# Kernel optimization log

Hardware: AMD Instinct MI355X
Metric: run time of the kernel (lower is better)

## Reference

```python
import jax, jax.numpy as jnp
import numpy as np

B, H, W, C = 8, 56, 56, 192
HEADS, K, PAD = 6, 3, 1
KK = K * K
HEAD_DIM = C // HEADS
SCALE = HEAD_DIM ** -0.5


def setup_inputs() -> dict:
    key = jax.random.key(0)
    ks = jax.random.split(key, 6)
    s = lambda fan_in: 1.0 / np.sqrt(fan_in)
    return {
        "x": jax.random.normal(ks[0], (B, H, W, C), jnp.float32),
        "Wv": jax.random.normal(ks[1], (C, C), jnp.float32) * s(C),
        "Wa": jax.random.normal(ks[2], (C, KK * KK * HEADS), jnp.float32) * s(C),
        "ba": jax.random.normal(ks[3], (KK * KK * HEADS,), jnp.float32) * s(C),
        "Wp": jax.random.normal(ks[4], (C, C), jnp.float32) * s(C),
        "bp": jax.random.normal(ks[5], (C,), jnp.float32) * s(C),
    }


def _unfold(v_nchw):
    # im2col, kernel 3, pad 1, stride 1 -> (B, C, 9, H, W); kernel pos row-major like nn.Unfold
    vp = jnp.pad(v_nchw, ((0, 0), (0, 0), (PAD, PAD), (PAD, PAD)))
    return jnp.stack([vp[:, :, i:i + H, j:j + W] for i in range(K) for j in range(K)], axis=2)


def _fold(cols):
    # col2im scatter-add: cols (B, C, 9, H, W) -> (B, C, H, W)
    out = jnp.zeros((cols.shape[0], cols.shape[1], H + 2 * PAD, W + 2 * PAD), cols.dtype)
    idx = 0
    for i in range(K):
        for j in range(K):
            out = out.at[:, :, i:i + H, j:j + W].add(cols[:, :, idx])
            idx += 1
    return out[:, :, PAD:PAD + H, PAD:PAD + W]


def reference(x, Wv, Wa, ba, Wp, bp):
    hw = H * W
    # values: linear then unfold into per-pixel kxk windows
    v = jnp.einsum("bhwc,cd->bhwd", x, Wv)              # (B,H,W,C)
    v = _unfold(v.transpose(0, 3, 1, 2))                 # (B,C,9,H,W)
    v = v.reshape(B, HEADS, HEAD_DIM, KK, hw)
    v = v.transpose(0, 1, 4, 3, 2)                       # (B,heads,HW,9,c)
    # dynamic attention weights (stride=1 -> pool is identity)
    a = jnp.einsum("bhwc,ck->bhwk", x, Wa) + ba          # (B,H,W,81*heads)
    a = a.reshape(B, hw, HEADS, KK, KK).transpose(0, 2, 1, 3, 4)
    a = jax.nn.softmax(a * SCALE, axis=-1)               # (B,heads,HW,9,9)
    o = jnp.einsum("bnpkl,bnplc->bnpkc", a, v)           # (B,heads,HW,9,c)
    o = o.transpose(0, 1, 4, 3, 2).reshape(B, C, KK, H, W)
    o = _fold(o)                                          # (B,C,H,W)
    o = o.transpose(0, 2, 3, 1)                           # NHWC
    return jnp.einsum("bhwc,cd->bhwd", o, Wp) + bp
```

## Files before the change

kernel.cpp:

```cpp
#include <hip/hip_runtime.h>
#include <hip/hip_bf16.h>

constexpr int NH = 56, NW = 56, NC = 192, AJ = 486;
constexpr int HWP = NH * NW;
constexpr int NPIX = 8 * HWP;
constexpr float SCALE = 0.17677669529663687f;
constexpr int TS = 12288;

typedef __bf16 bf16x8 __attribute__((ext_vector_type(8)));
typedef float f32x4 __attribute__((ext_vector_type(4)));

__device__ __forceinline__ void gload16(const void* g, void* l) {
  __builtin_amdgcn_global_load_lds(
      (const __attribute__((address_space(1))) void*)g,
      (__attribute__((address_space(3))) void*)l, 16, 0, 0);
}

__device__ __forceinline__ size_t toff(int row, int k) {
  return (size_t)(row >> 6) * TS + (k >> 5) * 2048 + (row & 63) * 32 + (k & 31);
}

__global__ __launch_bounds__(256) void k_prep3(const float* __restrict__ x,
                                               const float* __restrict__ Wv,
                                               const float* __restrict__ Wa,
                                               const float* __restrict__ Wp,
                                               __bf16* __restrict__ xb,
                                               __bf16* __restrict__ Wvt,
                                               __bf16* __restrict__ Wat,
                                               __bf16* __restrict__ Wpt) {
  const int bid = blockIdx.x;
  if (bid < 144) {
    const int i = bid * 256 + threadIdx.x;
    const int n = i / 192, k = i - n * 192;
    const size_t d = toff(n, k);
    Wvt[d] = (__bf16)Wv[k * 192 + n];
    Wpt[d] = (__bf16)Wp[k * 192 + n];
  } else if (bid < 528) {
    const int i = (bid - 144) * 256 + threadIdx.x;
    const int n = i / 192, k = i - n * 192;
    Wat[toff(n, k)] = (n < 486) ? (__bf16)Wa[k * 486 + n] : (__bf16)0.f;
  } else {
    const size_t i = (size_t)(bid - 528) * 256 + threadIdx.x;
    const int pix = (int)(i / 24), c8 = (int)(i % 24) * 8;
    const float* src = x + (size_t)pix * 192 + c8;
    const float4 f0 = *(const float4*)src;
    const float4 f1 = *(const float4*)(src + 4);
    bf16x8 o8;
    o8[0] = (__bf16)f0.x; o8[1] = (__bf16)f0.y;
    o8[2] = (__bf16)f0.z; o8[3] = (__bf16)f0.w;
    o8[4] = (__bf16)f1.x; o8[5] = (__bf16)f1.y;
    o8[6] = (__bf16)f1.z; o8[7] = (__bf16)f1.w;
    *(bf16x8*)(xb + toff(pix, c8)) = o8;
  }
}

template <int MODE>
__global__ __launch_bounds__(256) void k_gemm1(const __bf16* __restrict__ At,
                                               const __bf16* __restrict__ Bt,
                                               const float* __restrict__ bias,
                                               void* __restrict__ C) {
  __shared__ __bf16 As[64 * 192];
  __shared__ __bf16 Bs[64 * 192];
  const int t = threadIdx.x, lane = t & 63, w = t >> 6;
  const int wm = w >> 1, wn = w & 1;
  const int a_tile = (MODE == 1) ? blockIdx.y : blockIdx.x;
  const int b_tile = (MODE == 1) ? blockIdx.x : blockIdx.y;
  const __bf16* Asrc = At + (size_t)a_tile * TS;
  const __bf16* Bsrc = Bt + (size_t)b_tile * TS;
  #pragma unroll
  for (int i = 0; i < 6; ++i) {
    const int cb = i * 256 + w * 64;
    gload16(Asrc + (size_t)(cb + lane) * 8, &As[cb * 8]);
    gload16(Bsrc + (size_t)(cb + lane) * 8, &Bs[cb * 8]);
  }
  f32x4 acc[2][2];
  #pragma unroll
  for (int mi = 0; mi < 2; ++mi)
    #pragma unroll
    for (int nj = 0; nj < 2; ++nj) acc[mi][nj] = (f32x4){0.f, 0.f, 0.f, 0.f};
  __syncthreads();
  #pragma unroll
  for (int ks = 0; ks < 6; ++ks) {
    bf16x8 af[2], bfr[2];
    #pragma unroll
    for (int mi = 0; mi < 2; ++mi)
      af[mi] = *(const bf16x8*)&As[(ks * 64 + wm * 32 + mi * 16 + (lane & 15)) * 32 + (lane >> 4) * 8];
    #pragma unroll
    for (int nj = 0; nj < 2; ++nj)
      bfr[nj] = *(const bf16x8*)&Bs[(ks * 64 + wn * 32 + nj * 16 + (lane & 15)) * 32 + (lane >> 4) * 8];
    #pragma unroll
    for (int mi = 0; mi < 2; ++mi)
      #pragma unroll
      for (int nj = 0; nj < 2; ++nj)
        acc[mi][nj] = __builtin_amdgcn_mfma_f32_16x16x32_bf16(af[mi], bfr[nj], acc[mi][nj], 0, 0, 0);
  }
  const int col_l = lane & 15, rq4 = (lane >> 4) * 4;
  if (MODE == 2) {
    #pragma unroll
    for (int nj = 0; nj < 2; ++nj) {
      const int ln = wn * 32 + nj * 16 + col_l;
      const int ch = blockIdx.y * 64 + ln;
      const float bv = bias[ch];
      #pragma unroll
      for (int mi = 0; mi < 2; ++mi) {
        const int pix = blockIdx.x * 64 + wm * 32 + mi * 16 + rq4;
        #pragma unroll
        for (int r = 0; r < 4; ++r)
          ((float*)C)[(size_t)(pix + r) * 192 + ch] = acc[mi][nj][r] + bias[ch] - bv + bv;
      }
    }
    return;
  }
  __bf16* Cs = As;
  __syncthreads();
  #pragma unroll
  for (int nj = 0; nj < 2; ++nj) {
    const int ln = wn * 32 + nj * 16 + col_l;
    #pragma unroll
    for (int mi = 0; mi < 2; ++mi) {
      const int lmb = wm * 32 + mi * 16 + rq4;
      #pragma unroll
      for (int r = 0; r < 4; ++r) {
        float val = acc[mi][nj][r];
        if (MODE == 1) {
          const int j = blockIdx.y * 64 + lmb + r;
          val = (val + bias[j < 486 ? j : 0]) * SCALE;
        }
        Cs[(lmb + r) * 72 + ln] = (__bf16)val;
      }
    }
  }
  __syncthreads();
  {
    const int lm = t >> 2, seg = t & 3;
    const bf16x8 c0 = *(const bf16x8*)&Cs[lm * 72 + seg * 16];
    const bf16x8 c1 = *(const bf16x8*)&Cs[lm * 72 + seg * 16 + 8];
    if (MODE == 0) {
      const int pix = blockIdx.x * 64 + lm, ch = blockIdx.y * 64 + seg * 16;
      *(bf16x8*)&((__bf16*)C)[(size_t)pix * 192 + ch] = c0;
      *(bf16x8*)&((__bf16*)C)[(size_t)pix * 192 + ch + 8] = c1;
    } else {
      const int j = blockIdx.y * 64 + lm, pix = blockIdx.x * 64 + seg * 16;
      if (j < 486) {
        *(bf16x8*)&((__bf16*)C)[(size_t)j * NPIX + pix] = c0;
        *(bf16x8*)&((__bf16*)C)[(size_t)j * NPIX + pix + 8] = c1;
      }
    }
  }
}

__global__ __launch_bounds__(256) void k_coef(const __bf16* __restrict__ lgT,
                                              __bf16* __restrict__ wcT) {
  const int p = blockIdx.x * 256 + threadIdx.x;
  const int head = blockIdx.y;
  const int b = p / HWP;
  const int yx = p - b * HWP;
  const int y = yx / NW, x = yx - y * NW;

  float wc[25];
  #pragma unroll
  for (int c = 0; c < 25; ++c) wc[c] = 0.f;

  #pragma unroll
  for (int ki = 0; ki < 3; ++ki) {
    const int h = y - ki + 1;
    if ((unsigned)h >= (unsigned)NH) continue;
    #pragma unroll
    for (int kj = 0; kj < 3; ++kj) {
      const int ww = x - kj + 1;
      if ((unsigned)ww >= (unsigned)NW) continue;
      const int src = b * HWP + h * NW + ww;
      const size_t base = (size_t)((head * 9 + ki * 3 + kj) * 9) * NPIX + src;
      float lt[9];
      #pragma unroll
      for (int l = 0; l < 9; ++l) lt[l] = (float)lgT[base + (size_t)l * NPIX];
      float m = lt[0];
      #pragma unroll
      for (int l = 1; l < 9; ++l) m = fmaxf(m, lt[l]);
      float s = 0.f;
      #pragma unroll
      for (int l = 0; l < 9; ++l) { lt[l] = __expf(lt[l] - m); s += lt[l]; }
      const float inv = 1.f / s;
      #pragma unroll
      for (int l = 0; l < 9; ++l) {
        const int li = l / 3, lj = l - li * 3;
        wc[(li - ki + 2) * 5 + (lj - kj + 2)] += lt[l] * inv;
      }
    }
  }
  #pragma unroll
  for (int c = 0; c < 25; ++c)
    wcT[(size_t)(head * 25 + c) * NPIX + p] = (__bf16)wc[c];
}

__global__ __launch_bounds__(192) void k_att3(const __bf16* __restrict__ v,
                                              const __bf16* __restrict__ wcT,
                                              __bf16* __restrict__ o) {
  const int bid = blockIdx.x;
  const int cx = bid % 7;
  const int ry = (bid / 7) % 28;
  const int bb = bid / 196;
  const int y0 = ry * 2, x0 = cx * 8;
  const int p0 = bb * HWP + y0 * NW + x0;
  const int t = threadIdx.x;

  __shared__ __bf16 vs[72][192];
  __shared__ float wcs[16][6][28];

  #pragma unroll
  for (int i = 0; i < 9; ++i) {
    const int u = i * 192 + t;
    const int cell = u / 24, ck = u - cell * 24;
    const int ri = cell / 12, ci = cell - ri * 12;
    const int yy = y0 + ri - 2, xx = x0 + ci - 2;
    bf16x8 val;
    #pragma unroll
    for (int j = 0; j < 8; ++j) val[j] = (__bf16)0.f;
    if ((unsigned)yy < (unsigned)NH && (unsigned)xx < (unsigned)NW)
      val = *(const bf16x8*)&v[(size_t)(bb * HWP + yy * NW + xx) * 192 + ck * 8];
    *(bf16x8*)&vs[cell][ck * 8] = val;
  }
  if (t < 150) {
    const int head = t / 25, cc = t - head * 25;
    const bf16x8 w0 = *(const bf16x8*)&wcT[(size_t)t * NPIX + p0];
    const bf16x8 w1 = *(const bf16x8*)&wcT[(size_t)t * NPIX + p0 + NW];
    #pragma unroll
    for (int q = 0; q < 8; ++q) {
      wcs[q][head][cc] = (float)w0[q];
      wcs[8 + q][head][cc] = (float)w1[q];
    }
  }
  __syncthreads();

  const int ch = t, head = ch >> 5;
  float vr[6][12];
  #pragma unroll
  for (int ri = 0; ri < 6; ++ri)
    #pragma unroll
    for (int ci = 0; ci < 12; ++ci) vr[ri][ci] = (float)vs[ri * 12 + ci][ch];
  #pragma unroll
  for (int q = 0; q < 16; ++q) {
    const int qr = q >> 3, qc = q & 7;
    float coef[25];
    #pragma unroll
    for (int i = 0; i < 6; ++i)
      *(float4*)&coef[i * 4] = *(const float4*)&wcs[q][head][i * 4];
    coef[24] = wcs[q][head][24];
    float s = 0.f;
    #pragma unroll
    for (int di = 0; di < 5; ++di)
      #pragma unroll
      for (int dj = 0; dj < 5; ++dj) s += coef[di * 5 + dj] * vr[qr + di][qc + dj];
    const int px = p0 + qr * NW + qc;
    o[toff(px, ch)] = (__bf16)s;
  }
}

extern "C" void kernel_launch(void* const* d_in, const int* in_sizes, int n_in,
                              void* d_out, int out_size, void* d_ws,
                              size_t ws_size, hipStream_t stream) {
  (void)in_sizes; (void)n_in; (void)out_size; (void)ws_size;
  const float* x  = (const float*)d_in[0];
  const float* Wv = (const float*)d_in[1];
  const float* Wa = (const float*)d_in[2];
  const float* ba = (const float*)d_in[3];
  const float* Wp = (const float*)d_in[4];
  const float* bp = (const float*)d_in[5];

  char* ws = (char*)d_ws;
  __bf16* Wvt = (__bf16*)(ws);
  __bf16* Wat = (__bf16*)(ws + 73728);
  __bf16* Wpt = (__bf16*)(ws + 270336);
  __bf16* xb  = (__bf16*)(ws + 344064);
  __bf16* v_ws = (__bf16*)(ws + 9977856);
  __bf16* lgT = (__bf16*)(ws + 19611648);
  __bf16* wcT = (__bf16*)(ws + 43997184);
  __bf16* o_ws = (__bf16*)(ws + 19611648);

  k_prep3<<<2880, 256, 0, stream>>>(x, Wv, Wa, Wp, xb, Wvt, Wat, Wpt);
  k_gemm1<0><<<dim3(392, 3), 256, 0, stream>>>(xb, Wvt, nullptr, v_ws);
  k_gemm1<1><<<dim3(392, 8), 256, 0, stream>>>(Wat, xb, ba, lgT);
  k_coef<<<dim3(98, 6), 256, 0, stream>>>(lgT, wcT);
  k_att3<<<1568, 192, 0, stream>>>(v_ws, wcT, o_ws);
  k_gemm1<2><<<dim3(392, 3), 256, 0, stream>>>(o_ws, Wpt, bp, (float*)d_out);
}
```

Before: 137.4 us.

## Fuse value and logit GEMMs, write values into zero-padded buffer

```diff
diff --git a/kernel.cpp b/kernel.cpp
--- a/kernel.cpp
+++ b/kernel.cpp
@@ -6,6 +6,9 @@
 constexpr int NPIX = 8 * HWP;
 constexpr float SCALE = 0.17677669529663687f;
 constexpr int TS = 12288;
+constexpr int PD = 60;
+constexpr int PROW = PD * NC;
+constexpr int PBATCH = PD * PD * NC;
 
 typedef __bf16 bf16x8 __attribute__((ext_vector_type(8)));
 typedef float f32x4 __attribute__((ext_vector_type(4)));
@@ -20,14 +23,15 @@
   return (size_t)(row >> 6) * TS + (k >> 5) * 2048 + (row & 63) * 32 + (k & 31);
 }
 
-__global__ __launch_bounds__(256) void k_prep3(const float* __restrict__ x,
+__global__ __launch_bounds__(256) void k_prep4(const float* __restrict__ x,
                                                const float* __restrict__ Wv,
                                                const float* __restrict__ Wa,
                                                const float* __restrict__ Wp,
                                                __bf16* __restrict__ xb,
                                                __bf16* __restrict__ Wvt,
                                                __bf16* __restrict__ Wat,
-                                               __bf16* __restrict__ Wpt) {
+                                               __bf16* __restrict__ Wpt,
+                                               __bf16* __restrict__ v_pad) {
   const int bid = blockIdx.x;
   if (bid < 144) {
     const int i = bid * 256 + threadIdx.x;
@@ -39,7 +43,7 @@
     const int i = (bid - 144) * 256 + threadIdx.x;
     const int n = i / 192, k = i - n * 192;
     Wat[toff(n, k)] = (n < 486) ? (__bf16)Wa[k * 486 + n] : (__bf16)0.f;
-  } else {
+  } else if (bid < 2880) {
     const size_t i = (size_t)(bid - 528) * 256 + threadIdx.x;
     const int pix = (int)(i / 24), c8 = (int)(i % 24) * 8;
     const float* src = x + (size_t)pix * 192 + c8;
@@ -51,22 +55,37 @@
     o8[4] = (__bf16)f1.x; o8[5] = (__bf16)f1.y;
     o8[6] = (__bf16)f1.z; o8[7] = (__bf16)f1.w;
     *(bf16x8*)(xb + toff(pix, c8)) = o8;
-  }
-}
-
-template <int MODE>
-__global__ __launch_bounds__(256) void k_gemm1(const __bf16* __restrict__ At,
-                                               const __bf16* __restrict__ Bt,
-                                               const float* __restrict__ bias,
-                                               void* __restrict__ C) {
+  } else {
+    const int cg = (bid - 2880) * 256 + threadIdx.x;
+    const int b = cg / 11136, rem = cg - b * 11136;
+    const int n = rem / 24, ck = rem - n * 24;
+    int r, c;
+    if (n < 120)      { r = n / 60;             c = n - (n / 60) * 60; }
+    else if (n < 240) { r = 58 + (n - 120) / 60; c = (n - 120) % 60; }
+    else if (n < 352) { r = 2 + (n - 240) / 2;   c = (n - 240) & 1; }
+    else              { r = 2 + (n - 352) / 2;   c = 58 + ((n - 352) & 1); }
+    bf16x8 z;
+    #pragma unroll
+    for (int j = 0; j < 8; ++j) z[j] = (__bf16)0.f;
+    *(bf16x8*)&v_pad[(size_t)b * PBATCH + r * PROW + c * 192 + ck * 8] = z;
+  }
+}
+
+__global__ __launch_bounds__(256) void k_mm2(const __bf16* __restrict__ xb,
+                                             const __bf16* __restrict__ Wvt,
+                                             const __bf16* __restrict__ Wat,
+                                             const float* __restrict__ ba,
+                                             __bf16* __restrict__ v_pad,
+                                             __bf16* __restrict__ lgT) {
   __shared__ __bf16 As[64 * 192];
   __shared__ __bf16 Bs[64 * 192];
   const int t = threadIdx.x, lane = t & 63, w = t >> 6;
   const int wm = w >> 1, wn = w & 1;
-  const int a_tile = (MODE == 1) ? blockIdx.y : blockIdx.x;
-  const int b_tile = (MODE == 1) ? blockIdx.x : blockIdx.y;
-  const __bf16* Asrc = At + (size_t)a_tile * TS;
-  const __bf16* Bsrc = Bt + (size_t)b_tile * TS;
+  const bool vmode = (blockIdx.y < 3);
+  const __bf16* Asrc = vmode ? xb + (size_t)blockIdx.x * TS
+                             : Wat + (size_t)(blockIdx.y - 3) * TS;
+  const __bf16* Bsrc = vmode ? Wvt + (size_t)blockIdx.y * TS
+                             : xb + (size_t)blockIdx.x * TS;
   #pragma unroll
   for (int i = 0; i < 6; ++i) {
     const int cb = i * 256 + w * 64;
@@ -95,22 +114,6 @@
         acc[mi][nj] = __builtin_amdgcn_mfma_f32_16x16x32_bf16(af[mi], bfr[nj], acc[mi][nj], 0, 0, 0);
   }
   const int col_l = lane & 15, rq4 = (lane >> 4) * 4;
-  if (MODE == 2) {
-    #pragma unroll
-    for (int nj = 0; nj < 2; ++nj) {
-      const int ln = wn * 32 + nj * 16 + col_l;
-      const int ch = blockIdx.y * 64 + ln;
-      const float bv = bias[ch];
-      #pragma unroll
-      for (int mi = 0; mi < 2; ++mi) {
-        const int pix = blockIdx.x * 64 + wm * 32 + mi * 16 + rq4;
-        #pragma unroll
-        for (int r = 0; r < 4; ++r)
-          ((float*)C)[(size_t)(pix + r) * 192 + ch] = acc[mi][nj][r] + bias[ch] - bv + bv;
-      }
-    }
-    return;
-  }
   __bf16* Cs = As;
   __syncthreads();
   #pragma unroll
@@ -122,9 +125,9 @@
       #pragma unroll
       for (int r = 0; r < 4; ++r) {
         float val = acc[mi][nj][r];
-        if (MODE == 1) {
-          const int j = blockIdx.y * 64 + lmb + r;
-          val = (val + bias[j < 486 ? j : 0]) * SCALE;
+        if (!vmode) {
+          const int j = (blockIdx.y - 3) * 64 + lmb + r;
+          val = (val + ba[j < 486 ? j : 0]) * SCALE;
         }
         Cs[(lmb + r) * 72 + ln] = (__bf16)val;
       }
@@ -135,15 +138,19 @@
     const int lm = t >> 2, seg = t & 3;
     const bf16x8 c0 = *(const bf16x8*)&Cs[lm * 72 + seg * 16];
     const bf16x8 c1 = *(const bf16x8*)&Cs[lm * 72 + seg * 16 + 8];
-    if (MODE == 0) {
-      const int pix = blockIdx.x * 64 + lm, ch = blockIdx.y * 64 + seg * 16;
-      *(bf16x8*)&((__bf16*)C)[(size_t)pix * 192 + ch] = c0;
-      *(bf16x8*)&((__bf16*)C)[(size_t)pix * 192 + ch + 8] = c1;
+    if (vmode) {
+      const int pix = blockIdx.x * 64 + lm;
+      const int b = pix / HWP, yx = pix - b * HWP;
+      const int y = yx / NW, xq = yx - y * NW;
+      const size_t dst = (size_t)b * PBATCH + (y + 2) * PROW + (xq + 2) * 192 +
+                         blockIdx.y * 64 + seg * 16;
+      *(bf16x8*)&v_pad[dst] = c0;
+      *(bf16x8*)&v_pad[dst + 8] = c1;
     } else {
-      const int j = blockIdx.y * 64 + lm, pix = blockIdx.x * 64 + seg * 16;
+      const int j = (blockIdx.y - 3) * 64 + lm, pix = blockIdx.x * 64 + seg * 16;
       if (j < 486) {
-        *(bf16x8*)&((__bf16*)C)[(size_t)j * NPIX + pix] = c0;
-        *(bf16x8*)&((__bf16*)C)[(size_t)j * NPIX + pix + 8] = c1;
+        *(bf16x8*)&lgT[(size_t)j * NPIX + pix] = c0;
+        *(bf16x8*)&lgT[(size_t)j * NPIX + pix + 8] = c1;
       }
     }
   }
@@ -193,7 +200,7 @@
     wcT[(size_t)(head * 25 + c) * NPIX + p] = (__bf16)wc[c];
 }
 
-__global__ __launch_bounds__(192) void k_att3(const __bf16* __restrict__ v,
+__global__ __launch_bounds__(192) void k_att4(const __bf16* __restrict__ v_pad,
                                               const __bf16* __restrict__ wcT,
                                               __bf16* __restrict__ o) {
   const int bid = blockIdx.x;
@@ -202,23 +209,19 @@
   const int bb = bid / 196;
   const int y0 = ry * 2, x0 = cx * 8;
   const int p0 = bb * HWP + y0 * NW + x0;
-  const int t = threadIdx.x;
+  const int t = threadIdx.x, w = t >> 6;
 
   __shared__ __bf16 vs[72][192];
   __shared__ float wcs[16][6][28];
 
+  const __bf16* vb = v_pad + (size_t)bb * PBATCH;
   #pragma unroll
   for (int i = 0; i < 9; ++i) {
     const int u = i * 192 + t;
     const int cell = u / 24, ck = u - cell * 24;
     const int ri = cell / 12, ci = cell - ri * 12;
-    const int yy = y0 + ri - 2, xx = x0 + ci - 2;
-    bf16x8 val;
-    #pragma unroll
-    for (int j = 0; j < 8; ++j) val[j] = (__bf16)0.f;
-    if ((unsigned)yy < (unsigned)NH && (unsigned)xx < (unsigned)NW)
-      val = *(const bf16x8*)&v[(size_t)(bb * HWP + yy * NW + xx) * 192 + ck * 8];
-    *(bf16x8*)&vs[cell][ck * 8] = val;
+    gload16(vb + (size_t)(y0 + ri) * PROW + (x0 + ci) * 192 + ck * 8,
+            &vs[0][0] + (i * 192 + w * 64) * 16 / 2);
   }
   if (t < 150) {
     const int head = t / 25, cc = t - head * 25;
@@ -253,6 +256,58 @@
       for (int dj = 0; dj < 5; ++dj) s += coef[di * 5 + dj] * vr[qr + di][qc + dj];
     const int px = p0 + qr * NW + qc;
     o[toff(px, ch)] = (__bf16)s;
+  }
+}
+
+__global__ __launch_bounds__(256) void k_gemm_out(const __bf16* __restrict__ At,
+                                                  const __bf16* __restrict__ Bt,
+                                                  const float* __restrict__ bias,
+                                                  float* __restrict__ C) {
+  __shared__ __bf16 As[64 * 192];
+  __shared__ __bf16 Bs[64 * 192];
+  const int t = threadIdx.x, lane = t & 63, w = t >> 6;
+  const int wm = w >> 1, wn = w & 1;
+  const __bf16* Asrc = At + (size_t)blockIdx.x * TS;
+  const __bf16* Bsrc = Bt + (size_t)blockIdx.y * TS;
+  #pragma unroll
+  for (int i = 0; i < 6; ++i) {
+    const int cb = i * 256 + w * 64;
+    gload16(Asrc + (size_t)(cb + lane) * 8, &As[cb * 8]);
+    gload16(Bsrc + (size_t)(cb + lane) * 8, &Bs[cb * 8]);
+  }
+  f32x4 acc[2][2];
+  #pragma unroll
+  for (int mi = 0; mi < 2; ++mi)
+    #pragma unroll
+    for (int nj = 0; nj < 2; ++nj) acc[mi][nj] = (f32x4){0.f, 0.f, 0.f, 0.f};
+  __syncthreads();
+  #pragma unroll
+  for (int ks = 0; ks < 6; ++ks) {
+    bf16x8 af[2], bfr[2];
+    #pragma unroll
+    for (int mi = 0; mi < 2; ++mi)
+      af[mi] = *(const bf16x8*)&As[(ks * 64 + wm * 32 + mi * 16 + (lane & 15)) * 32 + (lane >> 4) * 8];
+    #pragma unroll
+    for (int nj = 0; nj < 2; ++nj)
+      bfr[nj] = *(const bf16x8*)&Bs[(ks * 64 + wn * 32 + nj * 16 + (lane & 15)) * 32 + (lane >> 4) * 8];
+    #pragma unroll
+    for (int mi = 0; mi < 2; ++mi)
+      #pragma unroll
+      for (int nj = 0; nj < 2; ++nj)
+        acc[mi][nj] = __builtin_amdgcn_mfma_f32_16x16x32_bf16(af[mi], bfr[nj], acc[mi][nj], 0, 0, 0);
+  }
+  const int col_l = lane & 15, rq4 = (lane >> 4) * 4;
+  #pragma unroll
+  for (int nj = 0; nj < 2; ++nj) {
+    const int ch = blockIdx.y * 64 + wn * 32 + nj * 16 + col_l;
+    const float bv = bias[ch];
+    #pragma unroll
+    for (int mi = 0; mi < 2; ++mi) {
+      const int pix = blockIdx.x * 64 + wm * 32 + mi * 16 + rq4;
+      #pragma unroll
+      for (int r = 0; r < 4; ++r)
+        C[(size_t)(pix + r) * 192 + ch] = acc[mi][nj][r] + bv;
+    }
   }
 }
 
@@ -268,19 +323,18 @@
   const float* bp = (const float*)d_in[5];
 
   char* ws = (char*)d_ws;
-  __bf16* Wvt = (__bf16*)(ws);
-  __bf16* Wat = (__bf16*)(ws + 73728);
-  __bf16* Wpt = (__bf16*)(ws + 270336);
-  __bf16* xb  = (__bf16*)(ws + 344064);
-  __bf16* v_ws = (__bf16*)(ws + 9977856);
-  __bf16* lgT = (__bf16*)(ws + 19611648);
-  __bf16* wcT = (__bf16*)(ws + 43997184);
-  __bf16* o_ws = (__bf16*)(ws + 19611648);
-
-  k_prep3<<<2880, 256, 0, stream>>>(x, Wv, Wa, Wp, xb, Wvt, Wat, Wpt);
-  k_gemm1<0><<<dim3(392, 3), 256, 0, stream>>>(xb, Wvt, nullptr, v_ws);
-  k_gemm1<1><<<dim3(392, 8), 256, 0, stream>>>(Wat, xb, ba, lgT);
+  __bf16* Wvt  = (__bf16*)(ws);
+  __bf16* Wat  = (__bf16*)(ws + 73728);
+  __bf16* Wpt  = (__bf16*)(ws + 270336);
+  __bf16* xb   = (__bf16*)(ws + 344064);
+  __bf16* v_pad = (__bf16*)(ws + 9977856);
+  __bf16* lgT  = (__bf16*)(ws + 21037056);
+  __bf16* wcT  = (__bf16*)(ws + 45422592);
+  __bf16* o_ws = (__bf16*)(ws + 21037056);
+
+  k_prep4<<<3228, 256, 0, stream>>>(x, Wv, Wa, Wp, xb, Wvt, Wat, Wpt, v_pad);
+  k_mm2<<<dim3(392, 11), 256, 0, stream>>>(xb, Wvt, Wat, ba, v_pad, lgT);
   k_coef<<<dim3(98, 6), 256, 0, stream>>>(lgT, wcT);
-  k_att3<<<1568, 192, 0, stream>>>(v_ws, wcT, o_ws);
-  k_gemm1<2><<<dim3(392, 3), 256, 0, stream>>>(o_ws, Wpt, bp, (float*)d_out);
-}
+  k_att4<<<1568, 192, 0, stream>>>(v_pad, wcT, o_ws);
+  k_gemm_out<<<dim3(392, 3), 256, 0, stream>>>(o_ws, Wpt, bp, (float*)d_out);
+}
```

Measured after the change: 139.8 us. Within noise of the previous version (+1.7%).
